# Optimization experiments

Hardware: AMD Instinct MI355X
Metric: run time of the kernel (lower is better)

## Reference

```python
import jax, jax.numpy as jnp
import numpy as np

N_NODES = 50000
N_EDGES = 800000
HID = 64
F_NODE = 64
F_EDGE = 16
DEC_H = 64
EPS = 1e-5


def setup_inputs() -> dict:
    key = jax.random.key(0)
    ks = jax.random.split(key, 16)
    inp = {}
    inp['x'] = jax.random.normal(ks[0], (N_NODES, F_NODE), dtype=jnp.float32)
    inp['edge_index'] = jax.random.randint(ks[1], (2, N_EDGES), 0, N_NODES, dtype=jnp.int32)
    inp['edge_attr'] = jax.random.normal(ks[2], (N_EDGES, F_EDGE), dtype=jnp.float32)
    # 3 GCN layers (F_NODE == HID so weights stack)
    inp['conv_w'] = jax.random.normal(ks[3], (3, HID, HID), dtype=jnp.float32) / np.sqrt(HID)
    inp['conv_b'] = jnp.zeros((3, HID), dtype=jnp.float32)
    inp['ln_g'] = jnp.ones((3, HID), dtype=jnp.float32)
    inp['ln_b'] = jnp.zeros((3, HID), dtype=jnp.float32)
    dec_in = 2 * HID + F_EDGE
    inp['dec_w1'] = jax.random.normal(ks[4], (dec_in, DEC_H), dtype=jnp.float32) / np.sqrt(dec_in)
    inp['dec_b1'] = jnp.zeros((DEC_H,), dtype=jnp.float32)
    inp['dec_w2'] = jax.random.normal(ks[5], (DEC_H, DEC_H // 2), dtype=jnp.float32) / np.sqrt(DEC_H)
    inp['dec_b2'] = jnp.zeros((DEC_H // 2,), dtype=jnp.float32)
    inp['dec_w3'] = jax.random.normal(ks[6], (DEC_H // 2, 1), dtype=jnp.float32) / np.sqrt(DEC_H // 2)
    inp['dec_b3'] = jnp.zeros((1,), dtype=jnp.float32)
    return inp


def _layer_norm(h, g, b):
    mu = jnp.mean(h, axis=-1, keepdims=True)
    var = jnp.mean(jnp.square(h - mu), axis=-1, keepdims=True)
    return (h - mu) * jax.lax.rsqrt(var + EPS) * g + b


def _forward(x, edge_index, edge_attr, conv_w, conv_b, ln_g, ln_b,
             dec_w1, dec_b1, dec_w2, dec_b2, dec_w3, dec_b3):
    n = x.shape[0]
    src, dst = edge_index[0], edge_index[1]
    # add self-loops (PyG GCNConv default)
    loop = jnp.arange(n, dtype=edge_index.dtype)
    src_sl = jnp.concatenate([src, loop])
    dst_sl = jnp.concatenate([dst, loop])
    # symmetric normalization: deg over target column (incl. self-loops)
    deg = jax.ops.segment_sum(jnp.ones_like(src_sl, dtype=x.dtype), dst_sl, num_segments=n)
    dinv = jnp.where(deg > 0, jax.lax.rsqrt(deg), 0.0)
    norm = dinv[src_sl] * dinv[dst_sl]  # (E+N,)

    h = x
    for l in range(conv_w.shape[0]):
        t = h @ conv_w[l]                                   # (N, H)
        msg = t[src_sl] * norm[:, None]                     # (E+N, H)
        agg = jax.ops.segment_sum(msg, dst_sl, num_segments=n) + conv_b[l]
        h = jax.nn.relu(_layer_norm(agg, ln_g[l], ln_b[l]))
        # dropout is identity at inference

    # edge decoder: concat(src_emb, dst_emb, edge_attr) -> MLP -> scalar
    z = jnp.concatenate([h[src], h[dst], edge_attr], axis=-1)  # (E, 2H+Fe)
    z = jax.nn.relu(z @ dec_w1 + dec_b1)
    z = jax.nn.relu(z @ dec_w2 + dec_b2)
    return (z @ dec_w3 + dec_b3).squeeze(-1)                   # (E,)


def reference(x, edge_index, edge_attr, conv_w, conv_b, ln_g, ln_b,
              dec_w1, dec_b1, dec_w2, dec_b2, dec_w3, dec_b3):
    return _forward(x, edge_index, edge_attr, conv_w, conv_b, ln_g, ln_b,
                    dec_w1, dec_b1, dec_w2, dec_b2, dec_w3, dec_b3)
```

## Files before the change

kernel.cpp:

```cpp
#include <hip/hip_runtime.h>
#include <hip/hip_fp16.h>

#define N_NODES 50000
#define N_EDGES 800000
#define HID 64
#define F_EDGE 16
#define LN_EPS 1e-5f
#define SCAN_BLOCKS ((N_NODES + 255) / 256)

typedef _Float16 h2n __attribute__((ext_vector_type(2)));

__device__ inline h2n to_n(__half2 v) {
    union { __half2 a; h2n b; } u; u.a = v; return u.b;
}
__device__ inline h2n pack2(float x, float y) {
    h2n r; r.x = (_Float16)x; r.y = (_Float16)y; return r;
}

__device__ inline float wave_sum64(float v) {
    #pragma unroll
    for (int o = 32; o > 0; o >>= 1) v += __shfl_xor(v, o, 64);
    return v;
}

__global__ void k_count(const int* __restrict__ dst, int* __restrict__ cnt) {
    int e = blockIdx.x * blockDim.x + threadIdx.x;
    if (e < N_EDGES) atomicAdd(&cnt[dst[e]], 1);
}

__global__ void k_scan1(const int* __restrict__ cnt, int* __restrict__ row_ptr,
                        int* __restrict__ bsum, float* __restrict__ dinv) {
    __shared__ int wsum[4];
    int tid = threadIdx.x, lane = tid & 63, w = tid >> 6;
    int i = blockIdx.x * 256 + tid;
    int v = (i < N_NODES) ? cnt[i] : 0;
    if (i < N_NODES) dinv[i] = rsqrtf((float)v + 1.0f);
    int isc = v;
    #pragma unroll
    for (int o = 1; o < 64; o <<= 1) {
        int n = __shfl_up(isc, o, 64);
        if (lane >= o) isc += n;
    }
    if (lane == 63) wsum[w] = isc;
    __syncthreads();
    int woff = 0;
    #pragma unroll
    for (int k = 0; k < 4; k++) woff += (k < w) ? wsum[k] : 0;
    if (i < N_NODES) row_ptr[i] = woff + isc - v;
    if (tid == 255) bsum[blockIdx.x] = woff + isc;
}

__global__ void k_scan2_prep(const int* __restrict__ bsum, int* __restrict__ boff,
                             const float* __restrict__ W1c, const float* __restrict__ W2,
                             __half2* __restrict__ w1cp, __half2* __restrict__ w2p) {
    __shared__ int wsum[4];
    int tid = threadIdx.x, lane = tid & 63, w = tid >> 6;
    int v = (tid < SCAN_BLOCKS) ? bsum[tid] : 0;
    int isc = v;
    #pragma unroll
    for (int o = 1; o < 64; o <<= 1) {
        int n = __shfl_up(isc, o, 64);
        if (lane >= o) isc += n;
    }
    if (lane == 63) wsum[w] = isc;
    __syncthreads();
    int woff = 0;
    #pragma unroll
    for (int k = 0; k < 4; k++) woff += (k < w) ? wsum[k] : 0;
    if (tid < SCAN_BLOCKS) boff[tid] = woff + isc - v;
    for (int i = tid; i < 8 * 64; i += 256) {
        int k2 = i >> 6, j = i & 63;
        w1cp[i] = __floats2half2_rn(W1c[(2 * k2) * 64 + j], W1c[(2 * k2 + 1) * 64 + j]);
    }
    for (int i = tid; i < 32 * 32; i += 256) {
        int k2 = i >> 5, j = i & 31;
        w2p[i] = __floats2half2_rn(W2[(2 * k2) * 32 + j], W2[(2 * k2 + 1) * 32 + j]);
    }
}

__global__ void k_scan3_xs(int* __restrict__ row_ptr, const int* __restrict__ boff,
                           int* __restrict__ cursor,
                           const float* __restrict__ x, const float* __restrict__ dinv,
                           __half* __restrict__ xs) {
    int i = blockIdx.x * blockDim.x + threadIdx.x;
    if (i < N_NODES) {
        int r = row_ptr[i] + boff[i >> 8];
        row_ptr[i] = r;
        cursor[i] = r;
    }
    if (i == 0) row_ptr[N_NODES] = N_EDGES;
    if (i < N_NODES * 64) xs[i] = __float2half_rn(x[i] * dinv[i >> 6]);
}

__global__ void k_fill(const int* __restrict__ src, const int* __restrict__ dst,
                       int* __restrict__ cursor, int* __restrict__ col) {
    int e = blockIdx.x * blockDim.x + threadIdx.x;
    if (e < N_EDGES) {
        int s = src[e], d = dst[e];
        int pos = atomicAdd(&cursor[d], 1);
        col[pos] = s;
    }
}

__device__ inline void row_acc(float4 raw, float m, float acc[8]) {
    const __half2* hp = (const __half2*)&raw;
    float2 f0 = __half22float2(hp[0]);
    float2 f1 = __half22float2(hp[1]);
    float2 f2 = __half22float2(hp[2]);
    float2 f3 = __half22float2(hp[3]);
    acc[0] = fmaf(f0.x, m, acc[0]); acc[1] = fmaf(f0.y, m, acc[1]);
    acc[2] = fmaf(f1.x, m, acc[2]); acc[3] = fmaf(f1.y, m, acc[3]);
    acc[4] = fmaf(f2.x, m, acc[4]); acc[5] = fmaf(f2.y, m, acc[5]);
    acc[6] = fmaf(f3.x, m, acc[6]); acc[7] = fmaf(f3.y, m, acc[7]);
}

__global__ void __launch_bounds__(256)
k_layer(const __half* __restrict__ xs_in, const float* __restrict__ dinv,
        const int* __restrict__ row_ptr, const int* __restrict__ col,
        const float* __restrict__ W, const float* __restrict__ cb,
        const float* __restrict__ gW, const float* __restrict__ bW,
        __half* __restrict__ xs_out, float* __restrict__ h_out) {
    __shared__ __align__(16) float tile[4][8 * 68];
    int tid = threadIdx.x;
    int wv = tid >> 6, lane = tid & 63;
    int base = (blockIdx.x * 4 + wv) * 8;
    if (base >= N_NODES) return;
    int g8 = lane >> 3;
    int c8 = lane & 7;
    int n = base + g8;
    const float4* x4 = (const float4*)xs_in;

    float acc[8];
    {
        float4 raw = x4[(size_t)n * 8 + c8];
        const __half2* hp = (const __half2*)&raw;
        float2 f0 = __half22float2(hp[0]);
        float2 f1 = __half22float2(hp[1]);
        float2 f2 = __half22float2(hp[2]);
        float2 f3 = __half22float2(hp[3]);
        acc[0] = f0.x; acc[1] = f0.y; acc[2] = f1.x; acc[3] = f1.y;
        acc[4] = f2.x; acc[5] = f2.y; acc[6] = f3.x; acc[7] = f3.y;
    }
    int beg = row_ptr[n], end = row_ptr[n + 1];
    int t = beg;
    int s0 = 0, s1 = 0, s2 = 0, s3 = 0;
    if (t < end) {
        int e1 = end - 1;
        s0 = col[t];
        s1 = col[min(t + 1, e1)];
        s2 = col[min(t + 2, e1)];
        s3 = col[min(t + 3, e1)];
    }
    while (t < end) {
        float m1 = (t + 1 < end) ? 1.0f : 0.0f;
        float m2 = (t + 2 < end) ? 1.0f : 0.0f;
        float m3 = (t + 3 < end) ? 1.0f : 0.0f;
        float4 r0 = x4[(size_t)s0 * 8 + c8];
        float4 r1 = x4[(size_t)s1 * 8 + c8];
        float4 r2 = x4[(size_t)s2 * 8 + c8];
        float4 r3 = x4[(size_t)s3 * 8 + c8];
        t += 4;
        if (t < end) {
            int e1 = end - 1;
            s0 = col[t];
            s1 = col[min(t + 1, e1)];
            s2 = col[min(t + 2, e1)];
            s3 = col[min(t + 3, e1)];
        }
        row_acc(r0, 1.0f, acc);
        row_acc(r1, m1, acc);
        row_acc(r2, m2, acc);
        row_acc(r3, m3, acc);
    }

    {
        float di = dinv[n];
        float4 y0, y1;
        y0.x = acc[0] * di; y0.y = acc[1] * di; y0.z = acc[2] * di; y0.w = acc[3] * di;
        y1.x = acc[4] * di; y1.y = acc[5] * di; y1.z = acc[6] * di; y1.w = acc[7] * di;
        float4* rowv = (float4*)&tile[wv][g8 * 68];
        rowv[(2 * c8)     ^ (g8 << 1)] = y0;
        rowv[(2 * c8 + 1) ^ (g8 << 1)] = y1;
    }

    float w[64];
    #pragma unroll
    for (int k = 0; k < 64; k++) w[k] = W[k * 64 + lane];
    float cbl = cb[lane], gl = gW[lane], bl = bW[lane];
    #pragma unroll
    for (int r = 0; r < 8; r++) {
        const float4* rw = (const float4*)&tile[wv][r * 68];
        float a = cbl;
        #pragma unroll
        for (int j = 0; j < 8; j++) {
            float4 p0 = rw[(2 * j)     ^ (r << 1)];
            float4 p1 = rw[(2 * j + 1) ^ (r << 1)];
            a = fmaf(p0.x, w[j * 8 + 0], a);
            a = fmaf(p0.y, w[j * 8 + 1], a);
            a = fmaf(p0.z, w[j * 8 + 2], a);
            a = fmaf(p0.w, w[j * 8 + 3], a);
            a = fmaf(p1.x, w[j * 8 + 4], a);
            a = fmaf(p1.y, w[j * 8 + 5], a);
            a = fmaf(p1.z, w[j * 8 + 6], a);
            a = fmaf(p1.w, w[j * 8 + 7], a);
        }
        float mu = wave_sum64(a) * (1.0f / 64.0f);
        float d = a - mu;
        float var = wave_sum64(d * d) * (1.0f / 64.0f);
        float y = fmaxf(fmaf(d * rsqrtf(var + LN_EPS), gl, bl), 0.0f);
        int nr = base + r;
        if (xs_out) {
            xs_out[nr * 64 + lane] = __float2half_rn(y * dinv[nr]);
        } else {
            h_out[nr * 64 + lane] = y;
        }
    }
}

__global__ void __launch_bounds__(256)
k_gemm_pq(const float* __restrict__ hin, const float* __restrict__ Wp,
          const float* __restrict__ bp, const float* __restrict__ Wq,
          __half* __restrict__ P, __half* __restrict__ Q) {
    int half_g = gridDim.x >> 1;
    bool isQ = (blockIdx.x >= half_g);
    const float* W = isQ ? Wq : Wp;
    __half* out = isQ ? Q : P;
    int lane = threadIdx.x & 63;
    int bid = isQ ? (blockIdx.x - half_g) : blockIdx.x;
    int wid = (bid * blockDim.x + threadIdx.x) >> 6;
    int nwaves = (half_g * blockDim.x) >> 6;
    float w[64];
    #pragma unroll
    for (int k = 0; k < 64; k++) w[k] = W[k * 64 + lane];
    float binit = isQ ? 0.0f : bp[lane];
    for (int row = wid; row < N_NODES; row += nwaves) {
        int r = __builtin_amdgcn_readfirstlane(row);
        const float* xr = hin + r * 64;
        float acc = binit;
        #pragma unroll
        for (int k = 0; k < 64; k++) acc = fmaf(xr[k], w[k], acc);
        out[r * 64 + lane] = __float2half_rn(acc);
    }
}

__global__ void __launch_bounds__(256)
k_decoder(const __half* __restrict__ P, const __half* __restrict__ Q,
          const int* __restrict__ src, const int* __restrict__ dst,
          const float* __restrict__ attr,
          const __half2* __restrict__ w1cp,
          const __half2* __restrict__ w2p, const float* __restrict__ b2,
          const float* __restrict__ W3, const float* __restrict__ b3,
          float* __restrict__ out) {
    int e = blockIdx.x * blockDim.x + threadIdx.x;
    if (e >= N_EDGES) return;
    int s = src[e], d = dst[e];

    const float4* ap = (const float4*)(attr + (size_t)e * 16);
    float4 av0 = ap[0], av1 = ap[1], av2 = ap[2], av3 = ap[3];
    h2n a2[8];
    a2[0] = pack2(av0.x, av0.y); a2[1] = pack2(av0.z, av0.w);
    a2[2] = pack2(av1.x, av1.y); a2[3] = pack2(av1.z, av1.w);
    a2[4] = pack2(av2.x, av2.y); a2[5] = pack2(av2.z, av2.w);
    a2[6] = pack2(av3.x, av3.y); a2[7] = pack2(av3.z, av3.w);

    float acc[64];
    const float4* Pp = (const float4*)(P + (size_t)s * 64);
    const float4* Qp = (const float4*)(Q + (size_t)d * 64);
    #pragma unroll
    for (int c = 0; c < 8; c++) {
        float4 pv = Pp[c], qv = Qp[c];
        const __half2* ph = (const __half2*)&pv;
        const __half2* qh = (const __half2*)&qv;
        #pragma unroll
        for (int u = 0; u < 4; u++) {
            float2 pf = __half22float2(ph[u]);
            float2 qf = __half22float2(qh[u]);
            acc[8 * c + 2 * u]     = pf.x + qf.x;
            acc[8 * c + 2 * u + 1] = pf.y + qf.y;
        }
    }

    #pragma unroll
    for (int k2 = 0; k2 < 8; k2++) {
        #pragma unroll
        for (int j = 0; j < 64; j++)
            acc[j] = __builtin_amdgcn_fdot2(a2[k2], to_n(w1cp[k2 * 64 + j]), acc[j], false);
    }

    h2n hh[32];
    #pragma unroll
    for (int k2 = 0; k2 < 32; k2++)
        hh[k2] = pack2(fmaxf(acc[2 * k2], 0.0f), fmaxf(acc[2 * k2 + 1], 0.0f));

    float acc2[32];
    #pragma unroll
    for (int j = 0; j < 32; j++) acc2[j] = b2[j];
    #pragma unroll
    for (int k2 = 0; k2 < 32; k2++) {
        #pragma unroll
        for (int j = 0; j < 32; j++)
            acc2[j] = __builtin_amdgcn_fdot2(hh[k2], to_n(w2p[k2 * 32 + j]), acc2[j], false);
    }

    float o = b3[0];
    #pragma unroll
    for (int j = 0; j < 32; j++)
        o = fmaf(fmaxf(acc2[j], 0.0f), W3[j], o);
    out[e] = o;
}

extern "C" void kernel_launch(void* const* d_in, const int* in_sizes, int n_in,
                              void* d_out, int out_size, void* d_ws, size_t ws_size,
                              hipStream_t stream) {
    const float* x      = (const float*)d_in[0];
    const int*   ei     = (const int*)d_in[1];
    const float* attr   = (const float*)d_in[2];
    const float* conv_w = (const float*)d_in[3];
    const float* conv_b = (const float*)d_in[4];
    const float* ln_g   = (const float*)d_in[5];
    const float* ln_b   = (const float*)d_in[6];
    const float* dw1    = (const float*)d_in[7];
    const float* db1    = (const float*)d_in[8];
    const float* dw2    = (const float*)d_in[9];
    const float* db2    = (const float*)d_in[10];
    const float* dw3    = (const float*)d_in[11];
    const float* db3    = (const float*)d_in[12];
    float* out = (float*)d_out;

    const int* src = ei;
    const int* dst = ei + N_EDGES;

    char* p = (char*)d_ws;
    float*   dinv    = (float*)p;   p += sizeof(float) * N_NODES;
    float*   h3      = (float*)p;   p += sizeof(float) * (size_t)N_NODES * 64;
    __half*  xs_a    = (__half*)p;  p += sizeof(__half) * (size_t)N_NODES * 64;
    __half*  xs_b    = (__half*)p;  p += sizeof(__half) * (size_t)N_NODES * 64;
    __half*  P_h     = (__half*)p;  p += sizeof(__half) * (size_t)N_NODES * 64;
    __half*  Q_h     = (__half*)p;  p += sizeof(__half) * (size_t)N_NODES * 64;
    int*     cnt     = (int*)p;     p += sizeof(int) * N_NODES;
    int*     cursor  = (int*)p;     p += sizeof(int) * N_NODES;
    int*     row_ptr = (int*)p;     p += sizeof(int) * (N_NODES + 1);
    int*     col     = (int*)p;     p += sizeof(int) * N_EDGES;
    int*     bsum    = (int*)p;     p += sizeof(int) * 256;
    int*     boff    = (int*)p;     p += sizeof(int) * 256;
    __half2* w1cp    = (__half2*)p; p += sizeof(__half2) * 8 * 64;
    __half2* w2p     = (__half2*)p; p += sizeof(__half2) * 32 * 32;

    const int nb_edges = (N_EDGES + 255) / 256;
    const int nb_elems = (N_NODES * 64 + 255) / 256;

    (void)hipMemsetAsync(cnt, 0, sizeof(int) * N_NODES, stream);
    k_count<<<nb_edges, 256, 0, stream>>>(dst, cnt);
    k_scan1<<<SCAN_BLOCKS, 256, 0, stream>>>(cnt, row_ptr, bsum, dinv);
    k_scan2_prep<<<1, 256, 0, stream>>>(bsum, boff, dw1 + 128 * 64, dw2, w1cp, w2p);
    k_scan3_xs<<<nb_elems, 256, 0, stream>>>(row_ptr, boff, cursor, x, dinv, xs_a);
    k_fill<<<nb_edges, 256, 0, stream>>>(src, dst, cursor, col);

    const int layer_blocks = (N_NODES / 8 + 3) / 4;
    const int gemm_blocks = 1024;

    k_layer<<<layer_blocks, 256, 0, stream>>>(
        xs_a, dinv, row_ptr, col, conv_w + 0 * 4096, conv_b + 0 * 64,
        ln_g + 0 * 64, ln_b + 0 * 64, xs_b, (float*)nullptr);
    k_layer<<<layer_blocks, 256, 0, stream>>>(
        xs_b, dinv, row_ptr, col, conv_w + 1 * 4096, conv_b + 1 * 64,
        ln_g + 1 * 64, ln_b + 1 * 64, xs_a, (float*)nullptr);
    k_layer<<<layer_blocks, 256, 0, stream>>>(
        xs_a, dinv, row_ptr, col, conv_w + 2 * 4096, conv_b + 2 * 64,
        ln_g + 2 * 64, ln_b + 2 * 64, (__half*)nullptr, h3);

    k_gemm_pq<<<2 * gemm_blocks, 256, 0, stream>>>(h3, dw1, db1, dw1 + 64 * 64, P_h, Q_h);

    k_decoder<<<nb_edges, 256, 0, stream>>>(
        P_h, Q_h, src, dst, attr, w1cp, w2p, db2, dw3, db3, out);
}
```

Measured before the change: 415.7 us.

## Fuse decoder P/Q projection into last GCN layer and merge scan kernels

```diff
diff --git a/kernel.cpp b/kernel.cpp
--- a/kernel.cpp
+++ b/kernel.cpp
@@ -29,8 +29,12 @@
 }
 
 __global__ void k_scan1(const int* __restrict__ cnt, int* __restrict__ row_ptr,
-                        int* __restrict__ bsum, float* __restrict__ dinv) {
+                        int* __restrict__ bsum, float* __restrict__ dinv,
+                        int* __restrict__ done, int* __restrict__ boff,
+                        const float* __restrict__ W1c, const float* __restrict__ W2,
+                        __half2* __restrict__ w1cp, __half2* __restrict__ w2p) {
     __shared__ int wsum[4];
+    __shared__ int amLast;
     int tid = threadIdx.x, lane = tid & 63, w = tid >> 6;
     int i = blockIdx.x * 256 + tid;
     int v = (i < N_NODES) ? cnt[i] : 0;
@@ -47,34 +51,39 @@
     #pragma unroll
     for (int k = 0; k < 4; k++) woff += (k < w) ? wsum[k] : 0;
     if (i < N_NODES) row_ptr[i] = woff + isc - v;
-    if (tid == 255) bsum[blockIdx.x] = woff + isc;
-}
-
-__global__ void k_scan2_prep(const int* __restrict__ bsum, int* __restrict__ boff,
-                             const float* __restrict__ W1c, const float* __restrict__ W2,
-                             __half2* __restrict__ w1cp, __half2* __restrict__ w2p) {
-    __shared__ int wsum[4];
-    int tid = threadIdx.x, lane = tid & 63, w = tid >> 6;
-    int v = (tid < SCAN_BLOCKS) ? bsum[tid] : 0;
-    int isc = v;
-    #pragma unroll
-    for (int o = 1; o < 64; o <<= 1) {
-        int n = __shfl_up(isc, o, 64);
-        if (lane >= o) isc += n;
-    }
-    if (lane == 63) wsum[w] = isc;
+    if (tid == 255) {
+        __hip_atomic_store(&bsum[blockIdx.x], woff + isc,
+                           __ATOMIC_RELEASE, __HIP_MEMORY_SCOPE_AGENT);
+        int prev = __hip_atomic_fetch_add(done, 1, __ATOMIC_ACQ_REL,
+                                          __HIP_MEMORY_SCOPE_AGENT);
+        amLast = (prev == SCAN_BLOCKS - 1) ? 1 : 0;
+    }
     __syncthreads();
-    int woff = 0;
-    #pragma unroll
-    for (int k = 0; k < 4; k++) woff += (k < w) ? wsum[k] : 0;
-    if (tid < SCAN_BLOCKS) boff[tid] = woff + isc - v;
-    for (int i = tid; i < 8 * 64; i += 256) {
-        int k2 = i >> 6, j = i & 63;
-        w1cp[i] = __floats2half2_rn(W1c[(2 * k2) * 64 + j], W1c[(2 * k2 + 1) * 64 + j]);
-    }
-    for (int i = tid; i < 32 * 32; i += 256) {
-        int k2 = i >> 5, j = i & 31;
-        w2p[i] = __floats2half2_rn(W2[(2 * k2) * 32 + j], W2[(2 * k2 + 1) * 32 + j]);
+    if (amLast) {
+        int v2 = (tid < SCAN_BLOCKS)
+                     ? __hip_atomic_load(&bsum[tid], __ATOMIC_ACQUIRE,
+                                         __HIP_MEMORY_SCOPE_AGENT)
+                     : 0;
+        int isc2 = v2;
+        #pragma unroll
+        for (int o = 1; o < 64; o <<= 1) {
+            int n = __shfl_up(isc2, o, 64);
+            if (lane >= o) isc2 += n;
+        }
+        if (lane == 63) wsum[w] = isc2;
+        __syncthreads();
+        int woff2 = 0;
+        #pragma unroll
+        for (int k = 0; k < 4; k++) woff2 += (k < w) ? wsum[k] : 0;
+        if (tid < SCAN_BLOCKS) boff[tid] = woff2 + isc2 - v2;
+        for (int j = tid; j < 8 * 64; j += 256) {
+            int k2 = j >> 6, c = j & 63;
+            w1cp[j] = __floats2half2_rn(W1c[(2 * k2) * 64 + c], W1c[(2 * k2 + 1) * 64 + c]);
+        }
+        for (int j = tid; j < 32 * 32; j += 256) {
+            int k2 = j >> 5, c = j & 31;
+            w2p[j] = __floats2half2_rn(W2[(2 * k2) * 32 + c], W2[(2 * k2 + 1) * 32 + c]);
+        }
     }
 }
 
@@ -119,7 +128,9 @@
         const int* __restrict__ row_ptr, const int* __restrict__ col,
         const float* __restrict__ W, const float* __restrict__ cb,
         const float* __restrict__ gW, const float* __restrict__ bW,
-        __half* __restrict__ xs_out, float* __restrict__ h_out) {
+        __half* __restrict__ xs_out,
+        const float* __restrict__ Wp, const float* __restrict__ bp,
+        __half* __restrict__ Pout, __half* __restrict__ Qout) {
     __shared__ __align__(16) float tile[4][8 * 68];
     int tid = threadIdx.x;
     int wv = tid >> 6, lane = tid & 63;
@@ -209,37 +220,58 @@
         float var = wave_sum64(d * d) * (1.0f / 64.0f);
         float y = fmaxf(fmaf(d * rsqrtf(var + LN_EPS), gl, bl), 0.0f);
         int nr = base + r;
-        if (xs_out) {
-            xs_out[nr * 64 + lane] = __float2half_rn(y * dinv[nr]);
+        if (Pout) {
+            int ch = (lane >> 2) ^ (r << 1);
+            tile[wv][r * 68 + 4 * ch + (lane & 3)] = y;
         } else {
-            h_out[nr * 64 + lane] = y;
-        }
-    }
-}
-
-__global__ void __launch_bounds__(256)
-k_gemm_pq(const float* __restrict__ hin, const float* __restrict__ Wp,
-          const float* __restrict__ bp, const float* __restrict__ Wq,
-          __half* __restrict__ P, __half* __restrict__ Q) {
-    int half_g = gridDim.x >> 1;
-    bool isQ = (blockIdx.x >= half_g);
-    const float* W = isQ ? Wq : Wp;
-    __half* out = isQ ? Q : P;
-    int lane = threadIdx.x & 63;
-    int bid = isQ ? (blockIdx.x - half_g) : blockIdx.x;
-    int wid = (bid * blockDim.x + threadIdx.x) >> 6;
-    int nwaves = (half_g * blockDim.x) >> 6;
-    float w[64];
-    #pragma unroll
-    for (int k = 0; k < 64; k++) w[k] = W[k * 64 + lane];
-    float binit = isQ ? 0.0f : bp[lane];
-    for (int row = wid; row < N_NODES; row += nwaves) {
-        int r = __builtin_amdgcn_readfirstlane(row);
-        const float* xr = hin + r * 64;
-        float acc = binit;
-        #pragma unroll
-        for (int k = 0; k < 64; k++) acc = fmaf(xr[k], w[k], acc);
-        out[r * 64 + lane] = __float2half_rn(acc);
+            xs_out[(size_t)nr * 64 + lane] = __float2half_rn(y * dinv[nr]);
+        }
+    }
+
+    if (Pout) {
+        #pragma unroll
+        for (int k = 0; k < 64; k++) w[k] = Wp[k * 64 + lane];
+        float bpl = bp[lane];
+        #pragma unroll
+        for (int r = 0; r < 8; r++) {
+            const float4* rw = (const float4*)&tile[wv][r * 68];
+            float a = bpl;
+            #pragma unroll
+            for (int j = 0; j < 8; j++) {
+                float4 p0 = rw[(2 * j)     ^ (r << 1)];
+                float4 p1 = rw[(2 * j + 1) ^ (r << 1)];
+                a = fmaf(p0.x, w[j * 8 + 0], a);
+                a = fmaf(p0.y, w[j * 8 + 1], a);
+                a = fmaf(p0.z, w[j * 8 + 2], a);
+                a = fmaf(p0.w, w[j * 8 + 3], a);
+                a = fmaf(p1.x, w[j * 8 + 4], a);
+                a = fmaf(p1.y, w[j * 8 + 5], a);
+                a = fmaf(p1.z, w[j * 8 + 6], a);
+                a = fmaf(p1.w, w[j * 8 + 7], a);
+            }
+            Pout[(size_t)(base + r) * 64 + lane] = __float2half_rn(a);
+        }
+        #pragma unroll
+        for (int k = 0; k < 64; k++) w[k] = Wp[(64 + k) * 64 + lane];
+        #pragma unroll
+        for (int r = 0; r < 8; r++) {
+            const float4* rw = (const float4*)&tile[wv][r * 68];
+            float a = 0.0f;
+            #pragma unroll
+            for (int j = 0; j < 8; j++) {
+                float4 p0 = rw[(2 * j)     ^ (r << 1)];
+                float4 p1 = rw[(2 * j + 1) ^ (r << 1)];
+                a = fmaf(p0.x, w[j * 8 + 0], a);
+                a = fmaf(p0.y, w[j * 8 + 1], a);
+                a = fmaf(p0.z, w[j * 8 + 2], a);
+                a = fmaf(p0.w, w[j * 8 + 3], a);
+                a = fmaf(p1.x, w[j * 8 + 4], a);
+                a = fmaf(p1.y, w[j * 8 + 5], a);
+                a = fmaf(p1.z, w[j * 8 + 6], a);
+                a = fmaf(p1.w, w[j * 8 + 7], a);
+            }
+            Qout[(size_t)(base + r) * 64 + lane] = __float2half_rn(a);
+        }
     }
 }
 
@@ -332,12 +364,12 @@
 
     char* p = (char*)d_ws;
     float*   dinv    = (float*)p;   p += sizeof(float) * N_NODES;
-    float*   h3      = (float*)p;   p += sizeof(float) * (size_t)N_NODES * 64;
     __half*  xs_a    = (__half*)p;  p += sizeof(__half) * (size_t)N_NODES * 64;
     __half*  xs_b    = (__half*)p;  p += sizeof(__half) * (size_t)N_NODES * 64;
     __half*  P_h     = (__half*)p;  p += sizeof(__half) * (size_t)N_NODES * 64;
     __half*  Q_h     = (__half*)p;  p += sizeof(__half) * (size_t)N_NODES * 64;
-    int*     cnt     = (int*)p;     p += sizeof(int) * N_NODES;
+    int*     cnt     = (int*)p;     p += sizeof(int) * (N_NODES + 1);
+    int*     done    = cnt + N_NODES;
     int*     cursor  = (int*)p;     p += sizeof(int) * N_NODES;
     int*     row_ptr = (int*)p;     p += sizeof(int) * (N_NODES + 1);
     int*     col     = (int*)p;     p += sizeof(int) * N_EDGES;
@@ -349,27 +381,27 @@
     const int nb_edges = (N_EDGES + 255) / 256;
     const int nb_elems = (N_NODES * 64 + 255) / 256;
 
-    (void)hipMemsetAsync(cnt, 0, sizeof(int) * N_NODES, stream);
+    (void)hipMemsetAsync(cnt, 0, sizeof(int) * (N_NODES + 1), stream);
     k_count<<<nb_edges, 256, 0, stream>>>(dst, cnt);
-    k_scan1<<<SCAN_BLOCKS, 256, 0, stream>>>(cnt, row_ptr, bsum, dinv);
-    k_scan2_prep<<<1, 256, 0, stream>>>(bsum, boff, dw1 + 128 * 64, dw2, w1cp, w2p);
+    k_scan1<<<SCAN_BLOCKS, 256, 0, stream>>>(cnt, row_ptr, bsum, dinv, done, boff,
+                                             dw1 + 128 * 64, dw2, w1cp, w2p);
     k_scan3_xs<<<nb_elems, 256, 0, stream>>>(row_ptr, boff, cursor, x, dinv, xs_a);
     k_fill<<<nb_edges, 256, 0, stream>>>(src, dst, cursor, col);
 
     const int layer_blocks = (N_NODES / 8 + 3) / 4;
-    const int gemm_blocks = 1024;
 
     k_layer<<<layer_blocks, 256, 0, stream>>>(
         xs_a, dinv, row_ptr, col, conv_w + 0 * 4096, conv_b + 0 * 64,
-        ln_g + 0 * 64, ln_b + 0 * 64, xs_b, (float*)nullptr);
+        ln_g + 0 * 64, ln_b + 0 * 64, xs_b,
+        (const float*)nullptr, (const float*)nullptr, (__half*)nullptr, (__half*)nullptr);
     k_layer<<<layer_blocks, 256, 0, stream>>>(
         xs_b, dinv, row_ptr, col, conv_w + 1 * 4096, conv_b + 1 * 64,
-        ln_g + 1 * 64, ln_b + 1 * 64, xs_a, (float*)nullptr);
+        ln_g + 1 * 64, ln_b + 1 * 64, xs_a,
+        (const float*)nullptr, (const float*)nullptr, (__half*)nullptr, (__half*)nullptr);
     k_layer<<<layer_blocks, 256, 0, stream>>>(
         xs_a, dinv, row_ptr, col, conv_w + 2 * 4096, conv_b + 2 * 64,
-        ln_g + 2 * 64, ln_b + 2 * 64, (__half*)nullptr, h3);
-
-    k_gemm_pq<<<2 * gemm_blocks, 256, 0, stream>>>(h3, dw1, db1, dw1 + 64 * 64, P_h, Q_h);
+        ln_g + 2 * 64, ln_b + 2 * 64, (__half*)nullptr,
+        dw1, db1, P_h, Q_h);
 
     k_decoder<<<nb_edges, 256, 0, stream>>>(
         P_h, Q_h, src, dst, attr, w1cp, w2p, db2, dw3, db3, out);
```

Result: slower. 468.8 us (+12.8%).
